# Kernel optimization log

Hardware: AMD Instinct MI355X
Metric: run time of the kernel (lower is better)

The kernel has to match this reference:

```python
import jax, jax.numpy as jnp
import numpy as np

N, E, D, A = 50000, 1_600_000, 32, 2
H1, C1, H2, C2 = 4, 16, 2, 32  # GATv2Conv(D,16,heads=4) -> 64; GATv2Conv(64,32,heads=2) -> 64


def setup_inputs() -> dict:
    key = jax.random.key(0)
    ks = jax.random.split(key, 16)

    def glorot(k, shape):
        fan = shape[0] + shape[-1]
        return jax.random.normal(k, shape, jnp.float32) * np.float32(np.sqrt(2.0 / fan))

    return {
        "x": jax.random.normal(ks[0], (N, D), jnp.float32),
        "edge_index": jax.random.randint(ks[1], (2, E), 0, N),
        "edge_attr": jax.random.normal(ks[2], (E, 2), jnp.float32),
        # GATv2 layer 1 (lin_l/lin_r with bias, lin_edge no bias, att [H,C], out bias)
        "w1_l": glorot(ks[3], (D, H1 * C1)), "b1_l": jnp.zeros((H1 * C1,), jnp.float32),
        "w1_r": glorot(ks[4], (D, H1 * C1)), "b1_r": jnp.zeros((H1 * C1,), jnp.float32),
        "w1_e": glorot(ks[5], (2, H1 * C1)),
        "att1": glorot(ks[6], (H1, C1)),
        "bias1": jnp.zeros((H1 * C1,), jnp.float32),
        # GATv2 layer 2
        "w2_l": glorot(ks[7], (H1 * C1, H2 * C2)), "b2_l": jnp.zeros((H2 * C2,), jnp.float32),
        "w2_r": glorot(ks[8], (H1 * C1, H2 * C2)), "b2_r": jnp.zeros((H2 * C2,), jnp.float32),
        "w2_e": glorot(ks[9], (2, H2 * C2)),
        "att2": glorot(ks[10], (H2, C2)),
        "bias2": jnp.zeros((H2 * C2,), jnp.float32),
        # heads
        "w_actor": glorot(ks[11], (H2 * C2, A)), "b_actor": jnp.zeros((A,), jnp.float32),
        "w_critic": glorot(ks[12], (H2 * C2, 1)), "b_critic": jnp.zeros((1,), jnp.float32),
        "log_std": jnp.zeros((A,), jnp.float32),
    }


def _gatv2(x, src, dst, eattr, Wl, bl, Wr, br, We, att, bias, H, C, n):
    # PyG GATv2Conv: message j->i with i = dst, j = src
    xl = (x @ Wl + bl).reshape(n, H, C)  # source-side transform (x_j)
    xr = (x @ Wr + br).reshape(n, H, C)  # target-side transform (x_i)
    ee = (eattr @ We).reshape(-1, H, C)  # per-edge embedding
    z = jax.nn.leaky_relu(xl[src] + xr[dst] + ee, 0.2)  # [Etot, H, C]
    logits = jnp.einsum('ehc,hc->eh', z, att)  # [Etot, H]
    # segment softmax over incoming edges of each dst node
    m = jax.ops.segment_max(logits, dst, num_segments=n)
    p = jnp.exp(logits - m[dst])
    denom = jax.ops.segment_sum(p, dst, num_segments=n)
    alpha = p / denom[dst]  # every node has a self-loop -> denom > 0
    msg = xl[src] * alpha[:, :, None]  # [Etot, H, C]
    out = jax.ops.segment_sum(msg, dst, num_segments=n)
    return out.reshape(n, H * C) + bias


def reference(x, edge_index, edge_attr,
              w1_l, b1_l, w1_r, b1_r, w1_e, att1, bias1,
              w2_l, b2_l, w2_r, b2_r, w2_e, att2, bias2,
              w_actor, b_actor, w_critic, b_critic, log_std):
    src, dst = edge_index[0], edge_index[1]
    # add_self_loops=True, fill_value='mean': self-loop edge_attr = mean of incoming edge_attr
    cnt = jax.ops.segment_sum(jnp.ones((edge_attr.shape[0],), x.dtype), dst, num_segments=N)
    sums = jax.ops.segment_sum(edge_attr, dst, num_segments=N)
    loop_attr = sums / jnp.maximum(cnt, 1.0)[:, None]
    loop = jnp.arange(N, dtype=src.dtype)
    src_f = jnp.concatenate([src, loop])
    dst_f = jnp.concatenate([dst, loop])
    ea = jnp.concatenate([edge_attr, loop_attr], axis=0)

    h = jax.nn.relu(_gatv2(x, src_f, dst_f, ea, w1_l, b1_l, w1_r, b1_r, w1_e, att1, bias1, H1, C1, N))
    h = jax.nn.relu(_gatv2(h, src_f, dst_f, ea, w2_l, b2_l, w2_r, b2_r, w2_e, att2, bias2, H2, C2, N))

    action_mean = jnp.tanh(h @ w_actor + b_actor)  # [N, A]
    value = h @ w_critic + b_critic               # [N, 1]
    std = jnp.exp(log_std)                        # [A]  (Normal(action_mean, std))
    return action_mean, std, value
```

## Files before the change

kernel.cpp:

```cpp
#include <hip/hip_runtime.h>
#include <math.h>

#define DIN   32
#define F1    64
#define F2    64

__device__ __forceinline__ unsigned bf16pack(float a, float b) {
    unsigned ua = __float_as_uint(a);
    unsigned ub = __float_as_uint(b);
    ua = (ua + 0x7FFFu + ((ua >> 16) & 1u)) >> 16;
    ub = (ub + 0x7FFFu + ((ub >> 16) & 1u)) >> 16;
    return ua | (ub << 16);
}

template <int K>
__device__ __forceinline__ void lin_lr_body(int bid,
        const float* __restrict__ x,
        const float* __restrict__ Wl, const float* __restrict__ bl,
        const float* __restrict__ Wr, const float* __restrict__ br,
        float* __restrict__ xl, float* __restrict__ xr, int n) {
    __shared__ float Ash[32][K + 4];
    __shared__ float Wsh[K][128];
    const int t = threadIdx.x;
    const int node0 = bid * 32;

    for (int idx = t; idx < 32 * (K / 4); idx += 256) {
        int m = idx / (K / 4), kq = idx % (K / 4);
        float4 v = make_float4(0.f, 0.f, 0.f, 0.f);
        if (node0 + m < n) v = ((const float4*)(x + (size_t)(node0 + m) * K))[kq];
        *(float4*)&Ash[m][kq * 4] = v;
    }
    for (int idx = t; idx < K * 32; idx += 256) {
        int k = idx / 32, j4 = idx % 32;
        float4 v = (j4 < 16) ? ((const float4*)(Wl + (size_t)k * 64))[j4]
                             : ((const float4*)(Wr + (size_t)k * 64))[j4 - 16];
        *(float4*)&Wsh[k][j4 * 4] = v;
    }
    __syncthreads();

    const int ty = t >> 4;
    const int tx = t & 15;
    float acc0[8], acc1[8];
#pragma unroll
    for (int j = 0; j < 8; j++) { acc0[j] = 0.f; acc1[j] = 0.f; }

#pragma unroll 4
    for (int k = 0; k < K; k++) {
        float a0 = Ash[ty * 2 + 0][k];
        float a1 = Ash[ty * 2 + 1][k];
        float4 w0 = *(const float4*)&Wsh[k][tx * 8];
        float4 w1 = *(const float4*)&Wsh[k][tx * 8 + 4];
        acc0[0] += a0 * w0.x; acc0[1] += a0 * w0.y;
        acc0[2] += a0 * w0.z; acc0[3] += a0 * w0.w;
        acc0[4] += a0 * w1.x; acc0[5] += a0 * w1.y;
        acc0[6] += a0 * w1.z; acc0[7] += a0 * w1.w;
        acc1[0] += a1 * w0.x; acc1[1] += a1 * w0.y;
        acc1[2] += a1 * w0.z; acc1[3] += a1 * w0.w;
        acc1[4] += a1 * w1.x; acc1[5] += a1 * w1.y;
        acc1[6] += a1 * w1.z; acc1[7] += a1 * w1.w;
    }

    const float* bsrc = (tx < 8) ? bl : br;
    int jb = (tx < 8) ? tx * 8 : (tx - 8) * 8;
    float4 b0 = ((const float4*)(bsrc + jb))[0];
    float4 b1 = ((const float4*)(bsrc + jb))[1];
    float* dst = (tx < 8) ? xl : xr;
#pragma unroll
    for (int m = 0; m < 2; m++) {
        int node = node0 + ty * 2 + m;
        if (node >= n) continue;
        const float* ac = (m == 0) ? acc0 : acc1;
        float4 o0, o1;
        o0.x = ac[0] + b0.x; o0.y = ac[1] + b0.y;
        o0.z = ac[2] + b0.z; o0.w = ac[3] + b0.w;
        o1.x = ac[4] + b1.x; o1.y = ac[5] + b1.y;
        o1.z = ac[6] + b1.z; o1.w = ac[7] + b1.w;
        ((float4*)(dst + (size_t)node * 64 + jb))[0] = o0;
        ((float4*)(dst + (size_t)node * 64 + jb))[1] = o1;
    }
}

__global__ __launch_bounds__(256, 2)
void fused_bcount_lin1(const int* __restrict__ dstr, int* __restrict__ cursor,
                       int* __restrict__ chunkoff, int* __restrict__ rank,
                       int E, int Ec, int NB, int gridLin,
                       const float* __restrict__ x,
                       const float* __restrict__ Wl, const float* __restrict__ bl,
                       const float* __restrict__ Wr, const float* __restrict__ br,
                       float* __restrict__ xl, float* __restrict__ xr, int n) {
    __shared__ int hist[256];
    if ((int)blockIdx.x < gridLin) {
        lin_lr_body<DIN>(blockIdx.x, x, Wl, bl, Wr, br, xl, xr, n);
        return;
    }
    const int blk = blockIdx.x - gridLin;
    const int t = threadIdx.x;
    hist[t] = 0;
    __syncthreads();
    const int s0 = blk * Ec, s1 = min(E, s0 + Ec);
    for (int e = s0 + t; e < s1; e += 256)
        rank[e] = atomicAdd(&hist[dstr[e] >> 8], 1);
    __syncthreads();
    if (t < NB) {
        int h = hist[t];
        chunkoff[blk * 256 + t] = h ? atomicAdd(&cursor[t], h) : 0;
    }
}

__global__ __launch_bounds__(512)
void scatter_buckets(const int* __restrict__ srcr, const int* __restrict__ dstr,
                     const float* __restrict__ ea, const int* __restrict__ rank,
                     const int* __restrict__ chunkoff,
                     int2* __restrict__ inter, int E, int Ec, int NB, int cap) {
    __shared__ int colsh[256];
    const int blk = blockIdx.x;
    const int t = threadIdx.x;
    if (t < 256) colsh[t] = (t < NB) ? (t * cap + chunkoff[blk * 256 + t]) : 0;
    __syncthreads();
    const int s0 = blk * Ec, s1 = min(E, s0 + Ec);
    for (int e = s0 + t; e < s1; e += 512) {
        int d = dstr[e];
        float2 v = ((const float2*)ea)[e];
        int2 r;
        r.x = srcr[e] | ((d & 255) << 24);
        r.y = (int)bf16pack(v.x, v.y);
        inter[colsh[d >> 8] + rank[e]] = r;
    }
}

__global__ __launch_bounds__(512)
void bucket_csr(const int2* __restrict__ inter, const int* __restrict__ cursor,
                int2* __restrict__ rse, float2* __restrict__ la2,
                int2* __restrict__ edges, int NB, int N, int cap) {
    __shared__ int sh[256];
    __shared__ int cur[256];
    __shared__ float las0[256];
    __shared__ float las1[256];
    const int b = blockIdx.x, t = threadIdx.x;
    const int bstart = b * cap;
    const int bend = bstart + cursor[b];

    if (t < 256) { sh[t] = 0; las0[t] = 0.f; las1[t] = 0.f; }
    __syncthreads();
    for (int pos = bstart + t; pos < bend; pos += 512) {
        int2 rec = inter[pos];
        int nd = ((unsigned)rec.x) >> 24;
        atomicAdd(&sh[nd], 1);
        atomicAdd(&las0[nd], __int_as_float(rec.y << 16));
        atomicAdd(&las1[nd], __int_as_float(rec.y & 0xFFFF0000));
    }
    __syncthreads();
    int v = 0;
    if (t < 256) v = sh[t];
    __syncthreads();
    if (t < 256) sh[t] = v;
    __syncthreads();
    for (int off = 1; off < 256; off <<= 1) {
        int x = (t >= off && t < 256) ? sh[t - off] : 0;
        __syncthreads();
        if (t < 256) sh[t] += x;
        __syncthreads();
    }
    if (t < 256) {
        int excl = sh[t] - v;
        cur[t] = excl;
        int node = b * 256 + t;
        if (node < N) {
            rse[node] = make_int2(bstart + excl, bstart + excl + v);
            float inv = v ? 1.0f / (float)v : 0.f;
            la2[node] = make_float2(las0[t] * inv, las1[t] * inv);
        }
    }
    __syncthreads();
    for (int pos = bstart + t; pos < bend; pos += 512) {
        int2 r = inter[pos];
        int k = atomicAdd(&cur[((unsigned)r.x) >> 24], 1);
        r.x &= 0x00FFFFFF;
        edges[bstart + k] = r;
    }
    int zend = (b + 1) * cap + ((b == NB - 1) ? 64 : 0);
    for (int pos = bend + t; pos < zend; pos += 512)
        edges[pos] = make_int2(0, 0);
}

__global__ __launch_bounds__(256, 2)
void lin_lr_tiled64(const float* __restrict__ x,
                    const float* __restrict__ Wl, const float* __restrict__ bl,
                    const float* __restrict__ Wr, const float* __restrict__ br,
                    float* __restrict__ xl, float* __restrict__ xr, int n) {
    lin_lr_body<F1>(blockIdx.x, x, Wl, bl, Wr, br, xl, xr, n);
}

template <int H, int C, bool FUSE_HEADS>
__global__ __launch_bounds__(256)
void gat_kernel(const float* __restrict__ xl, const float* __restrict__ xr,
                const int2* __restrict__ rse, const float2* __restrict__ la2,
                const int2* __restrict__ edges,
                const float* __restrict__ We, const float* __restrict__ att,
                const float* __restrict__ bias, float* __restrict__ hout,
                const float* __restrict__ wa, const float* __restrict__ ba,
                const float* __restrict__ wc, const float* __restrict__ bc,
                const float* __restrict__ ls, float* __restrict__ pout,
                int n) {
    constexpr int LPH = C / 4;
    if (FUSE_HEADS && blockIdx.x == 0 && threadIdx.x < 2)
        pout[(size_t)n * 2 + threadIdx.x] = expf(ls[threadIdx.x]);
    const int lane = threadIdx.x & 63;
    const int wid = (blockIdx.x * blockDim.x + threadIdx.x) >> 6;
    if (wid >= n) return;
    const int i = wid;
    const int g = lane >> 4;
    const int q = lane & 15;

    const float4* xl4 = (const float4*)xl;
    const float4 xri = ((const float4*)(xr + (size_t)i * 64))[q];
    const float4 we0 = ((const float4*)We)[q];
    const float4 we1 = ((const float4*)(We + 64))[q];
    float4 av = ((const float4*)att)[q];
    const float LOG2E = 1.4426950408889634f;
    av.x *= LOG2E; av.y *= LOG2E; av.z *= LOG2E; av.w *= LOG2E;

    float den = 0.f;
    float a0 = 0.f, a1 = 0.f, a2 = 0.f, a3 = 0.f;

    const int2 se = rse[i];
    const int e0 = se.x, e1 = se.y;
    const int r = (e1 - e0) & 7;

    if (r) {
        int2 h0 = edges[e0 + g];
        int2 h1 = edges[e0 + 4 + g];
        float4 xh0 = xl4[(h0.x << 4) + q];
        float4 xh1 = xl4[(h1.x << 4) + q];
        const bool v0 = g < r;
        const bool v1 = (4 + g) < r;
        float ea00 = v0 ? __int_as_float(h0.y << 16) : 0.f;
        float ea01 = v0 ? __int_as_float(h0.y & 0xFFFF0000) : 0.f;
        float ea10 = v1 ? __int_as_float(h1.y << 16) : 0.f;
        float ea11 = v1 ? __int_as_float(h1.y & 0xFFFF0000) : 0.f;
        float y0 = xh0.x + fmaf(ea00, we0.x, fmaf(ea01, we1.x, xri.x));
        float y1 = xh0.y + fmaf(ea00, we0.y, fmaf(ea01, we1.y, xri.y));
        float y2 = xh0.z + fmaf(ea00, we0.z, fmaf(ea01, we1.z, xri.z));
        float y3 = xh0.w + fmaf(ea00, we0.w, fmaf(ea01, we1.w, xri.w));
        float u0 = xh1.x + fmaf(ea10, we0.x, fmaf(ea11, we1.x, xri.x));
        float u1 = xh1.y + fmaf(ea10, we0.y, fmaf(ea11, we1.y, xri.y));
        float u2 = xh1.z + fmaf(ea10, we0.z, fmaf(ea11, we1.z, xri.z));
        float u3 = xh1.w + fmaf(ea10, we0.w, fmaf(ea11, we1.w, xri.w));
        y0 = fmaxf(y0, 0.2f * y0); u0 = fmaxf(u0, 0.2f * u0);
        y1 = fmaxf(y1, 0.2f * y1); u1 = fmaxf(u1, 0.2f * u1);
        y2 = fmaxf(y2, 0.2f * y2); u2 = fmaxf(u2, 0.2f * u2);
        y3 = fmaxf(y3, 0.2f * y3); u3 = fmaxf(u3, 0.2f * u3);
        float l0 = fmaf(y0, av.x, fmaf(y1, av.y, fmaf(y2, av.z, y3 * av.w)));
        float l1 = fmaf(u0, av.x, fmaf(u1, av.y, fmaf(u2, av.z, u3 * av.w)));
#pragma unroll
        for (int m = 1; m < LPH; m <<= 1) {
            l0 += __shfl_xor(l0, m, 64);
            l1 += __shfl_xor(l1, m, 64);
        }
        float p0 = v0 ? exp2f(l0) : 0.f;
        float p1 = v1 ? exp2f(l1) : 0.f;
        den += p0 + p1;
        a0 = fmaf(p0, xh0.x, fmaf(p1, xh1.x, a0));
        a1 = fmaf(p0, xh0.y, fmaf(p1, xh1.y, a1));
        a2 = fmaf(p0, xh0.z, fmaf(p1, xh1.z, a2));
        a3 = fmaf(p0, xh0.w, fmaf(p1, xh1.w, a3));
    }

    const int em = e0 + r;
    int2 rn0 = edges[em + g];
    int2 rn1 = edges[em + 4 + g];
    float4 xvn0 = xl4[(rn0.x << 4) + q];
    float4 xvn1 = xl4[(rn1.x << 4) + q];

    for (int eb = em; eb < e1; eb += 8) {
        int2 r0 = rn0, r1 = rn1;
        float4 xv0 = xvn0, xv1 = xvn1;
        rn0 = edges[eb + 8 + g];
        rn1 = edges[eb + 12 + g];
        xvn0 = xl4[(rn0.x << 4) + q];
        xvn1 = xl4[(rn1.x << 4) + q];

        float ea00 = __int_as_float(r0.y << 16);
        float ea01 = __int_as_float(r0.y & 0xFFFF0000);
        float ea10 = __int_as_float(r1.y << 16);
        float ea11 = __int_as_float(r1.y & 0xFFFF0000);

        float y0 = xv0.x + fmaf(ea00, we0.x, fmaf(ea01, we1.x, xri.x));
        float y1 = xv0.y + fmaf(ea00, we0.y, fmaf(ea01, we1.y, xri.y));
        float y2 = xv0.z + fmaf(ea00, we0.z, fmaf(ea01, we1.z, xri.z));
        float y3 = xv0.w + fmaf(ea00, we0.w, fmaf(ea01, we1.w, xri.w));
        float u0 = xv1.x + fmaf(ea10, we0.x, fmaf(ea11, we1.x, xri.x));
        float u1 = xv1.y + fmaf(ea10, we0.y, fmaf(ea11, we1.y, xri.y));
        float u2 = xv1.z + fmaf(ea10, we0.z, fmaf(ea11, we1.z, xri.z));
        float u3 = xv1.w + fmaf(ea10, we0.w, fmaf(ea11, we1.w, xri.w));
        y0 = fmaxf(y0, 0.2f * y0); u0 = fmaxf(u0, 0.2f * u0);
        y1 = fmaxf(y1, 0.2f * y1); u1 = fmaxf(u1, 0.2f * u1);
        y2 = fmaxf(y2, 0.2f * y2); u2 = fmaxf(u2, 0.2f * u2);
        y3 = fmaxf(y3, 0.2f * y3); u3 = fmaxf(u3, 0.2f * u3);
        float l0 = fmaf(y0, av.x, fmaf(y1, av.y, fmaf(y2, av.z, y3 * av.w)));
        float l1 = fmaf(u0, av.x, fmaf(u1, av.y, fmaf(u2, av.z, u3 * av.w)));
#pragma unroll
        for (int m = 1; m < LPH; m <<= 1) {
            l0 += __shfl_xor(l0, m, 64);
            l1 += __shfl_xor(l1, m, 64);
        }
        float p0 = exp2f(l0);
        float p1 = exp2f(l1);
        den += p0 + p1;
        a0 = fmaf(p0, xv0.x, fmaf(p1, xv1.x, a0));
        a1 = fmaf(p0, xv0.y, fmaf(p1, xv1.y, a1));
        a2 = fmaf(p0, xv0.z, fmaf(p1, xv1.z, a2));
        a3 = fmaf(p0, xv0.w, fmaf(p1, xv1.w, a3));
    }

#pragma unroll
    for (int m = 16; m < 64; m <<= 1) {
        den += __shfl_xor(den, m, 64);
        a0 += __shfl_xor(a0, m, 64);
        a1 += __shfl_xor(a1, m, 64);
        a2 += __shfl_xor(a2, m, 64);
        a3 += __shfl_xor(a3, m, 64);
    }

    const float2 lam = la2[i];
    const float4 xlv = xl4[(i << 4) + q];
    {
        float z0 = xlv.x + fmaf(lam.x, we0.x, fmaf(lam.y, we1.x, xri.x));
        float z1 = xlv.y + fmaf(lam.x, we0.y, fmaf(lam.y, we1.y, xri.y));
        float z2 = xlv.z + fmaf(lam.x, we0.z, fmaf(lam.y, we1.z, xri.z));
        float z3 = xlv.w + fmaf(lam.x, we0.w, fmaf(lam.y, we1.w, xri.w));
        z0 = fmaxf(z0, 0.2f * z0);
        z1 = fmaxf(z1, 0.2f * z1);
        z2 = fmaxf(z2, 0.2f * z2);
        z3 = fmaxf(z3, 0.2f * z3);
        float l = fmaf(z0, av.x, fmaf(z1, av.y, fmaf(z2, av.z, z3 * av.w)));
#pragma unroll
        for (int m = 1; m < LPH; m <<= 1) l += __shfl_xor(l, m, 64);
        float p = exp2f(l);
        den += p;
        a0 = fmaf(p, xlv.x, a0);
        a1 = fmaf(p, xlv.y, a1);
        a2 = fmaf(p, xlv.z, a2);
        a3 = fmaf(p, xlv.w, a3);
    }

    float rd = 1.0f / den;
    const float4 bv = ((const float4*)bias)[q];
    float4 o;
    o.x = fmaxf(fmaf(a0, rd, bv.x), 0.f);
    o.y = fmaxf(fmaf(a1, rd, bv.y), 0.f);
    o.z = fmaxf(fmaf(a2, rd, bv.z), 0.f);
    o.w = fmaxf(fmaf(a3, rd, bv.w), 0.f);

    if (!FUSE_HEADS) {
        if (g == 0) ((float4*)(hout + (size_t)i * 64))[q] = o;
    } else {
        float4 wa01 = ((const float4*)wa)[q * 2];
        float4 wa23 = ((const float4*)wa)[q * 2 + 1];
        float4 wcv  = ((const float4*)wc)[q];
        float d0 = o.x * wa01.x + o.y * wa01.z + o.z * wa23.x + o.w * wa23.z;
        float d1 = o.x * wa01.y + o.y * wa01.w + o.z * wa23.y + o.w * wa23.w;
        float d2 = o.x * wcv.x + o.y * wcv.y + o.z * wcv.z + o.w * wcv.w;
#pragma unroll
        for (int m = 1; m < 16; m <<= 1) {
            d0 += __shfl_xor(d0, m, 64);
            d1 += __shfl_xor(d1, m, 64);
            d2 += __shfl_xor(d2, m, 64);
        }
        if (lane == 0) {
            pout[(size_t)i * 2 + 0] = tanhf(d0 + ba[0]);
            pout[(size_t)i * 2 + 1] = tanhf(d1 + ba[1]);
            pout[(size_t)n * 2 + 2 + i] = d2 + bc[0];
        }
    }
}


extern "C" void kernel_launch(void* const* d_in, const int* in_sizes, int n_in,
                              void* d_out, int out_size, void* d_ws, size_t ws_size,
                              hipStream_t stream) {
    const float* x    = (const float*)d_in[0];
    const int*   ei   = (const int*)  d_in[1];
    const float* ea   = (const float*)d_in[2];
    const float* w1l  = (const float*)d_in[3];
    const float* b1l  = (const float*)d_in[4];
    const float* w1r  = (const float*)d_in[5];
    const float* b1r  = (const float*)d_in[6];
    const float* w1e  = (const float*)d_in[7];
    const float* att1 = (const float*)d_in[8];
    const float* bias1= (const float*)d_in[9];
    const float* w2l  = (const float*)d_in[10];
    const float* b2l  = (const float*)d_in[11];
    const float* w2r  = (const float*)d_in[12];
    const float* b2r  = (const float*)d_in[13];
    const float* w2e  = (const float*)d_in[14];
    const float* att2 = (const float*)d_in[15];
    const float* bias2= (const float*)d_in[16];
    const float* wa   = (const float*)d_in[17];
    const float* ba   = (const float*)d_in[18];
    const float* wc   = (const float*)d_in[19];
    const float* bc   = (const float*)d_in[20];
    const float* ls   = (const float*)d_in[21];

    const int N = in_sizes[0] / DIN;
    const int E = in_sizes[2] / 2;
    const int* srcr = ei;
    const int* dstr = ei + E;

    const int NB = (N + 255) >> 8;
    const int Ec = (E + 255) / 256;
    int cap = (E + NB - 1) / NB;
    cap = ((cap + cap / 4) + 63) & ~63;

    char* p = (char*)d_ws;
    auto alloc = [&](size_t bytes) -> void* {
        void* r = (void*)p;
        p += (bytes + 255) & ~(size_t)255;
        return r;
    };
    int*    cursor   = (int*)   alloc(256 * 4);
    int*    chunkoff = (int*)   alloc(256 * 256 * 4);
    int*    rank     = (int*)   alloc((size_t)E * 4);
    int2*   rse      = (int2*)  alloc((size_t)N * 8);
    float2* la2      = (float2*)alloc((size_t)N * 8);
    int2*   edges    = (int2*)  alloc(((size_t)NB * cap + 64) * 8);
    float*  xl       = (float*) alloc((size_t)N * F1 * 4);
    float*  xr       = (float*) alloc((size_t)N * F1 * 4);
    float*  h1       = (float*) alloc((size_t)N * F1 * 4);
    float*  h2       = (float*) alloc((size_t)N * F2 * 4);
    int2* inter = (int2*)h1;
    (void)ws_size; (void)n_in; (void)out_size;

    hipMemsetAsync(cursor, 0, 256 * 4, stream);

    const int TB = 256;
    int gridGemm = (N + 31) / 32;
    int gridWave = (N + 3) / 4;

    fused_bcount_lin1<<<gridGemm + 256, TB, 0, stream>>>(
        dstr, cursor, chunkoff, rank, E, Ec, NB, gridGemm,
        x, w1l, b1l, w1r, b1r, xl, xr, N);
    scatter_buckets<<<256, 512, 0, stream>>>(srcr, dstr, ea, rank, chunkoff,
                                             inter, E, Ec, NB, cap);
    bucket_csr<<<NB, 512, 0, stream>>>(inter, cursor, rse, la2, edges, NB, N, cap);

    gat_kernel<4, 16, false><<<gridWave, TB, 0, stream>>>(
        xl, xr, rse, la2, edges, w1e, att1, bias1, h1,
        nullptr, nullptr, nullptr, nullptr, nullptr, nullptr, N);
    lin_lr_tiled64<<<gridGemm, TB, 0, stream>>>(h1, w2l, b2l, w2r, b2r, xl, xr, N);
    gat_kernel<2, 32, true><<<gridWave, TB, 0, stream>>>(
        xl, xr, rse, la2, edges, w2e, att2, bias2, h2,
        wa, ba, wc, bc, ls, (float*)d_out, N);
}
```

Before: 309.8 us.

## Store source-side features in fp16 and compute self-loop means from sorted edges

The source-side transform xl is now written as half precision and converted back to float inside the GAT gather loop. This halves the bytes moved by the random per-edge neighbor gathers. Separately, bucket_csr drops its shared-memory float atomics for the self-loop attribute mean and instead has each node thread sum its contiguous sorted edges after the scatter. The trade-offs are reduced precision of xl and a serial per-node loop.

```diff
diff --git a/kernel.cpp b/kernel.cpp
--- a/kernel.cpp
+++ b/kernel.cpp
@@ -1,4 +1,5 @@
 #include <hip/hip_runtime.h>
+#include <hip/hip_fp16.h>
 #include <math.h>
 
 #define DIN   32
@@ -18,7 +19,7 @@
         const float* __restrict__ x,
         const float* __restrict__ Wl, const float* __restrict__ bl,
         const float* __restrict__ Wr, const float* __restrict__ br,
-        float* __restrict__ xl, float* __restrict__ xr, int n) {
+        __half* __restrict__ xl, float* __restrict__ xr, int n) {
     __shared__ float Ash[32][K + 4];
     __shared__ float Wsh[K][128];
     const int t = threadIdx.x;
@@ -64,19 +65,30 @@
     int jb = (tx < 8) ? tx * 8 : (tx - 8) * 8;
     float4 b0 = ((const float4*)(bsrc + jb))[0];
     float4 b1 = ((const float4*)(bsrc + jb))[1];
-    float* dst = (tx < 8) ? xl : xr;
 #pragma unroll
     for (int m = 0; m < 2; m++) {
         int node = node0 + ty * 2 + m;
         if (node >= n) continue;
         const float* ac = (m == 0) ? acc0 : acc1;
-        float4 o0, o1;
-        o0.x = ac[0] + b0.x; o0.y = ac[1] + b0.y;
-        o0.z = ac[2] + b0.z; o0.w = ac[3] + b0.w;
-        o1.x = ac[4] + b1.x; o1.y = ac[5] + b1.y;
-        o1.z = ac[6] + b1.z; o1.w = ac[7] + b1.w;
-        ((float4*)(dst + (size_t)node * 64 + jb))[0] = o0;
-        ((float4*)(dst + (size_t)node * 64 + jb))[1] = o1;
+        float o0 = ac[0] + b0.x, o1 = ac[1] + b0.y;
+        float o2 = ac[2] + b0.z, o3 = ac[3] + b0.w;
+        float o4 = ac[4] + b1.x, o5 = ac[5] + b1.y;
+        float o6 = ac[6] + b1.z, o7 = ac[7] + b1.w;
+        if (tx < 8) {
+            __half2 h0 = __floats2half2_rn(o0, o1);
+            __half2 h1 = __floats2half2_rn(o2, o3);
+            __half2 h2 = __floats2half2_rn(o4, o5);
+            __half2 h3 = __floats2half2_rn(o6, o7);
+            uint4 pk;
+            pk.x = *(unsigned*)&h0; pk.y = *(unsigned*)&h1;
+            pk.z = *(unsigned*)&h2; pk.w = *(unsigned*)&h3;
+            *((uint4*)(xl + (size_t)node * 64 + jb)) = pk;
+        } else {
+            float4 f0 = make_float4(o0, o1, o2, o3);
+            float4 f1 = make_float4(o4, o5, o6, o7);
+            ((float4*)(xr + (size_t)node * 64 + jb))[0] = f0;
+            ((float4*)(xr + (size_t)node * 64 + jb))[1] = f1;
+        }
     }
 }
 
@@ -87,7 +99,7 @@
                        const float* __restrict__ x,
                        const float* __restrict__ Wl, const float* __restrict__ bl,
                        const float* __restrict__ Wr, const float* __restrict__ br,
-                       float* __restrict__ xl, float* __restrict__ xr, int n) {
+                       __half* __restrict__ xl, float* __restrict__ xr, int n) {
     __shared__ int hist[256];
     if ((int)blockIdx.x < gridLin) {
         lin_lr_body<DIN>(blockIdx.x, x, Wl, bl, Wr, br, xl, xr, n);
@@ -134,26 +146,19 @@
                 int2* __restrict__ edges, int NB, int N, int cap) {
     __shared__ int sh[256];
     __shared__ int cur[256];
-    __shared__ float las0[256];
-    __shared__ float las1[256];
     const int b = blockIdx.x, t = threadIdx.x;
     const int bstart = b * cap;
     const int bend = bstart + cursor[b];
 
-    if (t < 256) { sh[t] = 0; las0[t] = 0.f; las1[t] = 0.f; }
-    __syncthreads();
-    for (int pos = bstart + t; pos < bend; pos += 512) {
-        int2 rec = inter[pos];
-        int nd = ((unsigned)rec.x) >> 24;
-        atomicAdd(&sh[nd], 1);
-        atomicAdd(&las0[nd], __int_as_float(rec.y << 16));
-        atomicAdd(&las1[nd], __int_as_float(rec.y & 0xFFFF0000));
-    }
-    __syncthreads();
-    int v = 0;
-    if (t < 256) v = sh[t];
-    __syncthreads();
-    if (t < 256) sh[t] = v;
+    if (t < 256) sh[t] = 0;
+    __syncthreads();
+    for (int pos = bstart + t; pos < bend; pos += 512)
+        atomicAdd(&sh[((unsigned)inter[pos].x) >> 24], 1);
+    __syncthreads();
+    int cnt_v = 0, myrs = 0;
+    if (t < 256) cnt_v = sh[t];
+    __syncthreads();
+    if (t < 256) sh[t] = cnt_v;
     __syncthreads();
     for (int off = 1; off < 256; off <<= 1) {
         int x = (t >= off && t < 256) ? sh[t - off] : 0;
@@ -162,14 +167,11 @@
         __syncthreads();
     }
     if (t < 256) {
-        int excl = sh[t] - v;
+        int excl = sh[t] - cnt_v;
         cur[t] = excl;
+        myrs = bstart + excl;
         int node = b * 256 + t;
-        if (node < N) {
-            rse[node] = make_int2(bstart + excl, bstart + excl + v);
-            float inv = v ? 1.0f / (float)v : 0.f;
-            la2[node] = make_float2(las0[t] * inv, las1[t] * inv);
-        }
+        if (node < N) rse[node] = make_int2(myrs, myrs + cnt_v);
     }
     __syncthreads();
     for (int pos = bstart + t; pos < bend; pos += 512) {
@@ -181,19 +183,33 @@
     int zend = (b + 1) * cap + ((b == NB - 1) ? 64 : 0);
     for (int pos = bend + t; pos < zend; pos += 512)
         edges[pos] = make_int2(0, 0);
+    __syncthreads();
+    if (t < 256) {
+        int node = b * 256 + t;
+        if (node < N) {
+            float s0 = 0.f, s1 = 0.f;
+            for (int pos = myrs; pos < myrs + cnt_v; pos++) {
+                int2 rec = edges[pos];
+                s0 += __int_as_float(rec.y << 16);
+                s1 += __int_as_float(rec.y & 0xFFFF0000);
+            }
+            float inv = cnt_v ? 1.0f / (float)cnt_v : 0.f;
+            la2[node] = make_float2(s0 * inv, s1 * inv);
+        }
+    }
 }
 
 __global__ __launch_bounds__(256, 2)
 void lin_lr_tiled64(const float* __restrict__ x,
                     const float* __restrict__ Wl, const float* __restrict__ bl,
                     const float* __restrict__ Wr, const float* __restrict__ br,
-                    float* __restrict__ xl, float* __restrict__ xr, int n) {
+                    __half* __restrict__ xl, float* __restrict__ xr, int n) {
     lin_lr_body<F1>(blockIdx.x, x, Wl, bl, Wr, br, xl, xr, n);
 }
 
 template <int H, int C, bool FUSE_HEADS>
 __global__ __launch_bounds__(256)
-void gat_kernel(const float* __restrict__ xl, const float* __restrict__ xr,
+void gat_kernel(const __half* __restrict__ xl, const float* __restrict__ xr,
                 const int2* __restrict__ rse, const float2* __restrict__ la2,
                 const int2* __restrict__ edges,
                 const float* __restrict__ We, const float* __restrict__ att,
@@ -212,7 +228,12 @@
     const int g = lane >> 4;
     const int q = lane & 15;
 
-    const float4* xl4 = (const float4*)xl;
+    const uint2* xlh = (const uint2*)xl;
+    auto h4tof4 = [](uint2 h) -> float4 {
+        float2 lo = __half22float2(*(__half2*)&h.x);
+        float2 hi = __half22float2(*(__half2*)&h.y);
+        return make_float4(lo.x, lo.y, hi.x, hi.y);
+    };
     const float4 xri = ((const float4*)(xr + (size_t)i * 64))[q];
     const float4 we0 = ((const float4*)We)[q];
     const float4 we1 = ((const float4*)(We + 64))[q];
@@ -230,8 +251,8 @@
     if (r) {
         int2 h0 = edges[e0 + g];
         int2 h1 = edges[e0 + 4 + g];
-        float4 xh0 = xl4[(h0.x << 4) + q];
-        float4 xh1 = xl4[(h1.x << 4) + q];
+        float4 xh0 = h4tof4(xlh[(h0.x << 4) + q]);
+        float4 xh1 = h4tof4(xlh[(h1.x << 4) + q]);
         const bool v0 = g < r;
         const bool v1 = (4 + g) < r;
         float ea00 = v0 ? __int_as_float(h0.y << 16) : 0.f;
@@ -269,16 +290,17 @@
     const int em = e0 + r;
     int2 rn0 = edges[em + g];
     int2 rn1 = edges[em + 4 + g];
-    float4 xvn0 = xl4[(rn0.x << 4) + q];
-    float4 xvn1 = xl4[(rn1.x << 4) + q];
+    uint2 xpn0 = xlh[(rn0.x << 4) + q];
+    uint2 xpn1 = xlh[(rn1.x << 4) + q];
 
     for (int eb = em; eb < e1; eb += 8) {
         int2 r0 = rn0, r1 = rn1;
-        float4 xv0 = xvn0, xv1 = xvn1;
+        float4 xv0 = h4tof4(xpn0);
+        float4 xv1 = h4tof4(xpn1);
         rn0 = edges[eb + 8 + g];
         rn1 = edges[eb + 12 + g];
-        xvn0 = xl4[(rn0.x << 4) + q];
-        xvn1 = xl4[(rn1.x << 4) + q];
+        xpn0 = xlh[(rn0.x << 4) + q];
+        xpn1 = xlh[(rn1.x << 4) + q];
 
         float ea00 = __int_as_float(r0.y << 16);
         float ea01 = __int_as_float(r0.y & 0xFFFF0000);
@@ -323,7 +345,7 @@
     }
 
     const float2 lam = la2[i];
-    const float4 xlv = xl4[(i << 4) + q];
+    const float4 xlv = h4tof4(xlh[(i << 4) + q]);
     {
         float z0 = xlv.x + fmaf(lam.x, we0.x, fmaf(lam.y, we1.x, xri.x));
         float z1 = xlv.y + fmaf(lam.x, we0.y, fmaf(lam.y, we1.y, xri.y));
@@ -424,7 +446,7 @@
     int2*   rse      = (int2*)  alloc((size_t)N * 8);
     float2* la2      = (float2*)alloc((size_t)N * 8);
     int2*   edges    = (int2*)  alloc(((size_t)NB * cap + 64) * 8);
-    float*  xl       = (float*) alloc((size_t)N * F1 * 4);
+    __half* xl       = (__half*)alloc((size_t)N * F1 * 2);
     float*  xr       = (float*) alloc((size_t)N * F1 * 4);
     float*  h1       = (float*) alloc((size_t)N * F1 * 4);
     float*  h2       = (float*) alloc((size_t)N * F2 * 4);
```

New measurement: 293.0 us. -5.4%, faster.
